# Optimization experiments

Measured on AMD Instinct MI355X. Metric: run time of the kernel, lower is better.

## Reference

```python
import jax, jax.numpy as jnp
import numpy as np

B, CTRL, KEY, MEMU = 64, 512, 64, 16384  # batch, controller_size, key_size(=memory_unit_size), memory_units
EPS_COS = 1e-8   # torch F.cosine_similarity default eps
EPS_NORM = 1e-16


def setup_inputs() -> dict:
    key = jax.random.key(0)
    ks = jax.random.split(key, 16)
    controller_state = jax.random.normal(ks[0], (B, CTRL), jnp.float32)
    pw = jax.random.uniform(ks[1], (B, MEMU), jnp.float32)
    prev_weights = pw / jnp.sum(pw, axis=1, keepdims=True)  # valid attention weights
    memory = jax.random.normal(ks[2], (B, MEMU, KEY), jnp.float32)
    def lin(k, out_d, in_d):
        kw, kb = jax.random.split(k)
        scale = 1.0 / np.sqrt(in_d)
        return (jax.random.normal(kw, (out_d, in_d), jnp.float32) * scale,
                jax.random.normal(kb, (out_d,), jnp.float32) * 0.01)
    key_W, key_b = lin(ks[3], KEY, CTRL)
    ks_W, ks_b = lin(ks[4], 1, CTRL)
    ig_W, ig_b = lin(ks[5], 1, CTRL)
    sw_W, sw_b = lin(ks[6], 3, CTRL)
    sf_W, sf_b = lin(ks[7], 1, CTRL)
    wd_W, wd_b = lin(ks[8], KEY, CTRL)
    return dict(controller_state=controller_state, prev_weights=prev_weights, memory=memory,
                key_W=key_W, key_b=key_b, ks_W=ks_W, ks_b=ks_b, ig_W=ig_W, ig_b=ig_b,
                sw_W=sw_W, sw_b=sw_b, sf_W=sf_W, sf_b=sf_b, wd_W=wd_W, wd_b=wd_b)


def _ntm_head(cs, prev_w, mem, key_W, key_b, ks_W, ks_b, ig_W, ig_b, sw_W, sw_b, sf_W, sf_b, wd_W, wd_b):
    k = cs @ key_W.T + key_b                       # (B, KEY)
    b = jax.nn.softplus(cs @ ks_W.T + ks_b)        # (B, 1) key strength
    g = jax.nn.sigmoid(cs @ ig_W.T + ig_b)         # (B, 1) interpolation gate
    s = jax.nn.softmax(cs @ sw_W.T + sw_b, axis=-1)  # (B, 3) shift weights
    y = 1.0 + jax.nn.softplus(cs @ sf_W.T + sf_b)  # (B, 1) sharpen factor
    # content addressing: softmax(b * cosine_sim(key, memory rows))
    dots = jnp.einsum('bmw,bw->bm', mem, k)        # (B, MEMU)
    denom = jnp.maximum(jnp.linalg.norm(mem, axis=2) * jnp.linalg.norm(k, axis=1, keepdims=True), EPS_COS)
    w_c = jax.nn.softmax(b * (dots / denom), axis=1)
    # interpolation with previous weights
    w_i = g * w_c + (1.0 - g) * prev_w             # (B, MEMU)
    # 3-tap circular shift (cross-correlation, matching the padded conv1d)
    shifted = (s[:, 0:1] * jnp.roll(w_i, 1, axis=1)
               + s[:, 1:2] * w_i
               + s[:, 2:3] * jnp.roll(w_i, -1, axis=1))
    # sharpen + normalize
    sharp = shifted ** y
    w = sharp / (jnp.sum(sharp, axis=1, keepdims=True) + EPS_NORM)
    data = jnp.einsum('bm,bmw->bw', w, mem)        # read mode
    return w, data


def reference(controller_state, prev_weights, memory, key_W, key_b, ks_W, ks_b,
              ig_W, ig_b, sw_W, sw_b, sf_W, sf_b, wd_W, wd_b):
    return _ntm_head(controller_state, prev_weights, memory, key_W, key_b, ks_W, ks_b,
                     ig_W, ig_b, sw_W, sw_b, sf_W, sf_b, wd_W, wd_b)
```

## Files before the change

kernel.cpp:

```cpp
#include <hip/hip_runtime.h>
#include <math.h>

#define B    64
#define CTRL 512
#define KEY  64
#define MEMU 16384

__device__ __forceinline__ float softplusf(float x) {
    return x > 20.f ? x : log1pf(expf(x));
}

__global__ __launch_bounds__(256) void k1_scalars(
    const float* __restrict__ cs,
    const float* __restrict__ key_W, const float* __restrict__ key_b,
    const float* __restrict__ ks_W,  const float* __restrict__ ks_b,
    const float* __restrict__ ig_W,  const float* __restrict__ ig_b,
    const float* __restrict__ sw_W,  const float* __restrict__ sw_b,
    const float* __restrict__ sf_W,  const float* __restrict__ sf_b,
    float* __restrict__ ws_k, float* __restrict__ ws_scal)
{
    __shared__ float cs_s[CTRL];
    __shared__ float k_s[KEY];
    __shared__ float h_s[8];
    const int b = blockIdx.x;
    const int t = threadIdx.x;
    for (int i = t; i < CTRL; i += 256) cs_s[i] = cs[b * CTRL + i];
    __syncthreads();
    const int wave = t >> 6, lane = t & 63;
    for (int o = wave; o < 70; o += 4) {
        const float* W; float bias;
        if (o < 64)       { W = key_W + o * CTRL;      bias = key_b[o]; }
        else if (o == 64) { W = ks_W;                  bias = ks_b[0]; }
        else if (o == 65) { W = ig_W;                  bias = ig_b[0]; }
        else if (o < 69)  { W = sw_W + (o - 66) * CTRL; bias = sw_b[o - 66]; }
        else              { W = sf_W;                  bias = sf_b[0]; }
        float d = 0.f;
        for (int j = lane; j < CTRL; j += 64) d += cs_s[j] * W[j];
        #pragma unroll
        for (int off = 32; off >= 1; off >>= 1) d += __shfl_xor(d, off, 64);
        if (lane == 0) {
            float r = d + bias;
            if (o < 64) { k_s[o] = r; ws_k[b * KEY + o] = r; }
            else        h_s[o - 64] = r;
        }
    }
    __syncthreads();
    if (wave == 0) {
        float kv = k_s[lane];
        float sq = kv * kv;
        #pragma unroll
        for (int off = 32; off >= 1; off >>= 1) sq += __shfl_xor(sq, off, 64);
        if (lane == 0) {
            float knorm = sqrtf(sq);
            float beta = softplusf(h_s[0]);
            float g    = 1.f / (1.f + expf(-h_s[1]));
            float m3   = fmaxf(fmaxf(h_s[2], h_s[3]), h_s[4]);
            float e0 = expf(h_s[2] - m3), e1 = expf(h_s[3] - m3), e2 = expf(h_s[4] - m3);
            float inv3 = 1.f / (e0 + e1 + e2);
            float y = 1.f + softplusf(h_s[5]);
            float* sc = ws_scal + b * 8;
            sc[0] = beta; sc[1] = g;
            sc[2] = e0 * inv3; sc[3] = e1 * inv3; sc[4] = e2 * inv3;
            sc[5] = y; sc[6] = knorm;
        }
    }
}

__global__ __launch_bounds__(256) void k2_scores(
    const float* __restrict__ mem,
    const float* __restrict__ ws_k, const float* __restrict__ ws_scal,
    float* __restrict__ ws_e, float* __restrict__ ws_pe)
{
    const int b = blockIdx.y;
    const int chunk = blockIdx.x;
    const int t = threadIdx.x;
    const float beta  = ws_scal[b * 8 + 0];
    const float knorm = ws_scal[b * 8 + 6];
    float kk[KEY];
    #pragma unroll
    for (int j = 0; j < KEY; ++j) kk[j] = ws_k[b * KEY + j];

    float esum = 0.f;
    #pragma unroll
    for (int i = 0; i < 4; ++i) {
        const int m = chunk * 1024 + i * 256 + t;
        const float4* rp = (const float4*)(mem + ((size_t)b * MEMU + m) * KEY);
        float dot = 0.f, sq = 0.f;
        #pragma unroll
        for (int q = 0; q < 16; ++q) {
            float4 v = rp[q];
            dot += v.x * kk[4*q+0] + v.y * kk[4*q+1] + v.z * kk[4*q+2] + v.w * kk[4*q+3];
            sq  += v.x * v.x + v.y * v.y + v.z * v.z + v.w * v.w;
        }
        const float denom = fmaxf(sqrtf(sq) * knorm, 1e-8f);
        const float e = expf(beta * (dot / denom) - beta);
        ws_e[b * MEMU + m] = e;
        esum += e;
    }
    __shared__ float red[4];
    #pragma unroll
    for (int off = 32; off >= 1; off >>= 1) esum += __shfl_xor(esum, off, 64);
    if ((t & 63) == 0) red[t >> 6] = esum;
    __syncthreads();
    if (t == 0) ws_pe[b * 16 + chunk] = red[0] + red[1] + red[2] + red[3];
}

__global__ __launch_bounds__(256) void k4_sharp(
    const float* __restrict__ pw,
    const float* __restrict__ ws_e, const float* __restrict__ ws_pe,
    const float* __restrict__ ws_scal,
    float* __restrict__ ws_sharp, float* __restrict__ ws_ps)
{
    const int b = blockIdx.y, chunk = blockIdx.x, t = threadIdx.x;
    float sum_e = 0.f;
    #pragma unroll
    for (int i = 0; i < 16; ++i) sum_e += ws_pe[b * 16 + i];
    const float inv_e = 1.f / sum_e;
    const float g  = ws_scal[b*8+1];
    const float s0 = ws_scal[b*8+2], s1 = ws_scal[b*8+3], s2 = ws_scal[b*8+4];
    const float y  = ws_scal[b*8+5];
    const float cg = 1.f - g;
    const float* eb = ws_e + b * MEMU;
    const float* pb = pw   + b * MEMU;

    float ssum = 0.f;
    #pragma unroll
    for (int i = 0; i < 8; ++i) {
        const int m  = chunk * 2048 + i * 256 + t;
        const int mm = (m + MEMU - 1) & (MEMU - 1);
        const int mp = (m + 1) & (MEMU - 1);
        const float wim = g * eb[mm] * inv_e + cg * pb[mm];
        const float wi0 = g * eb[m ] * inv_e + cg * pb[m ];
        const float wip = g * eb[mp] * inv_e + cg * pb[mp];
        const float sh  = s0 * wim + s1 * wi0 + s2 * wip;
        const float sp  = expf(y * logf(sh));
        ws_sharp[b * MEMU + m] = sp;
        ssum += sp;
    }
    __shared__ float red[4];
    #pragma unroll
    for (int off = 32; off >= 1; off >>= 1) ssum += __shfl_xor(ssum, off, 64);
    if ((t & 63) == 0) red[t >> 6] = ssum;
    __syncthreads();
    if (t == 0) ws_ps[b * 8 + chunk] = red[0] + red[1] + red[2] + red[3];
}

__global__ __launch_bounds__(256) void k6_wout(
    const float* __restrict__ ws_sharp, const float* __restrict__ ws_ps,
    float* __restrict__ out)
{
    const int b = blockIdx.y, chunk = blockIdx.x, t = threadIdx.x;
    float ss = 0.f;
    #pragma unroll
    for (int i = 0; i < 8; ++i) ss += ws_ps[b * 8 + i];
    const float inv = 1.f / (ss + 1e-16f);
    #pragma unroll
    for (int i = 0; i < 8; ++i) {
        const int m = chunk * 2048 + i * 256 + t;
        out[b * MEMU + m] = ws_sharp[b * MEMU + m] * inv;
    }
}

__global__ __launch_bounds__(256) void k7_data(
    const float* __restrict__ mem, const float* __restrict__ out_w,
    float* __restrict__ ws_pd)
{
    const int b = blockIdx.y, chunk = blockIdx.x;
    const int t = threadIdx.x, wave = t >> 6, lane = t & 63;
    const int r0 = chunk * 256 + wave * 64;
    const float* wb = out_w + b * MEMU;
    const float* mb = mem + (size_t)b * MEMU * KEY;
    float acc = 0.f;
    #pragma unroll 4
    for (int i = 0; i < 64; ++i) {
        const int r = r0 + i;
        acc += wb[r] * mb[(size_t)r * KEY + lane];
    }
    __shared__ float red[4][64];
    red[wave][lane] = acc;
    __syncthreads();
    if (t < 64) {
        const float s = red[0][t] + red[1][t] + red[2][t] + red[3][t];
        ws_pd[(b * 64 + chunk) * 64 + t] = s;
    }
}

__global__ __launch_bounds__(64) void k8_reduce(
    const float* __restrict__ ws_pd, float* __restrict__ out)
{
    const int b = blockIdx.x, j = threadIdx.x;
    float s = 0.f;
    #pragma unroll 8
    for (int c = 0; c < 64; ++c) s += ws_pd[(b * 64 + c) * 64 + j];
    out[(size_t)B * MEMU + b * KEY + j] = s;
}

extern "C" void kernel_launch(void* const* d_in, const int* in_sizes, int n_in,
                              void* d_out, int out_size, void* d_ws, size_t ws_size,
                              hipStream_t stream) {
    (void)in_sizes; (void)n_in; (void)out_size; (void)ws_size;
    const float* cs    = (const float*)d_in[0];
    const float* pw    = (const float*)d_in[1];
    const float* mem   = (const float*)d_in[2];
    const float* key_W = (const float*)d_in[3];
    const float* key_b = (const float*)d_in[4];
    const float* ks_W  = (const float*)d_in[5];
    const float* ks_b  = (const float*)d_in[6];
    const float* ig_W  = (const float*)d_in[7];
    const float* ig_b  = (const float*)d_in[8];
    const float* sw_W  = (const float*)d_in[9];
    const float* sw_b  = (const float*)d_in[10];
    const float* sf_W  = (const float*)d_in[11];
    const float* sf_b  = (const float*)d_in[12];
    float* out = (float*)d_out;
    float* ws  = (float*)d_ws;

    float* ws_k     = ws;
    float* ws_scal  = ws_k + B * KEY;
    float* ws_e     = ws_scal + B * 8;
    float* ws_sharp = ws_e + (size_t)B * MEMU;
    float* ws_pe    = ws_sharp + (size_t)B * MEMU;
    float* ws_ps    = ws_pe + B * 16;
    float* ws_pd    = ws_ps + B * 8;

    k1_scalars<<<dim3(B), dim3(256), 0, stream>>>(cs, key_W, key_b, ks_W, ks_b,
                                                  ig_W, ig_b, sw_W, sw_b, sf_W, sf_b,
                                                  ws_k, ws_scal);
    k2_scores<<<dim3(16, B), dim3(256), 0, stream>>>(mem, ws_k, ws_scal, ws_e, ws_pe);
    k4_sharp<<<dim3(8, B), dim3(256), 0, stream>>>(pw, ws_e, ws_pe, ws_scal, ws_sharp, ws_ps);
    k6_wout<<<dim3(8, B), dim3(256), 0, stream>>>(ws_sharp, ws_ps, out);
    k7_data<<<dim3(64, B), dim3(256), 0, stream>>>(mem, out, ws_pd);
    k8_reduce<<<dim3(B), dim3(64), 0, stream>>>(ws_pd, out);
}
```

Baseline: 125.6 us.

## Fuse weight normalization into data read kernel with float4 memory loads

```diff
diff --git a/kernel.cpp b/kernel.cpp
--- a/kernel.cpp
+++ b/kernel.cpp
@@ -145,43 +145,53 @@
     if (t == 0) ws_ps[b * 8 + chunk] = red[0] + red[1] + red[2] + red[3];
 }
 
-__global__ __launch_bounds__(256) void k6_wout(
+__global__ __launch_bounds__(256) void k7_data(
+    const float* __restrict__ mem,
     const float* __restrict__ ws_sharp, const float* __restrict__ ws_ps,
-    float* __restrict__ out)
-{
-    const int b = blockIdx.y, chunk = blockIdx.x, t = threadIdx.x;
+    float* __restrict__ out_w, float* __restrict__ ws_pd)
+{
+    const int b = blockIdx.y, chunk = blockIdx.x;
+    const int t = threadIdx.x, wv = t >> 6, lane = t & 63;
+    __shared__ float w_lds[256];
+    __shared__ float red[4][64];
+
     float ss = 0.f;
     #pragma unroll
     for (int i = 0; i < 8; ++i) ss += ws_ps[b * 8 + i];
     const float inv = 1.f / (ss + 1e-16f);
-    #pragma unroll
-    for (int i = 0; i < 8; ++i) {
-        const int m = chunk * 2048 + i * 256 + t;
-        out[b * MEMU + m] = ws_sharp[b * MEMU + m] * inv;
-    }
-}
-
-__global__ __launch_bounds__(256) void k7_data(
-    const float* __restrict__ mem, const float* __restrict__ out_w,
-    float* __restrict__ ws_pd)
-{
-    const int b = blockIdx.y, chunk = blockIdx.x;
-    const int t = threadIdx.x, wave = t >> 6, lane = t & 63;
-    const int r0 = chunk * 256 + wave * 64;
-    const float* wb = out_w + b * MEMU;
-    const float* mb = mem + (size_t)b * MEMU * KEY;
-    float acc = 0.f;
-    #pragma unroll 4
-    for (int i = 0; i < 64; ++i) {
-        const int r = r0 + i;
-        acc += wb[r] * mb[(size_t)r * KEY + lane];
-    }
-    __shared__ float red[4][64];
-    red[wave][lane] = acc;
+
+    const int m0 = chunk * 256;
+    const float wval = ws_sharp[b * MEMU + m0 + t] * inv;
+    out_w[b * MEMU + m0 + t] = wval;
+    w_lds[t] = wval;
+    __syncthreads();
+
+    const float* mb = mem + ((size_t)b * MEMU + m0 + wv * 64) * KEY;
+    const int rsub = lane >> 4;
+    const int c4   = (lane & 15) * 4;
+    float4 acc = make_float4(0.f, 0.f, 0.f, 0.f);
+    #pragma unroll
+    for (int s = 0; s < 16; ++s) {
+        const int r = s * 4 + rsub;
+        const float4 v = *(const float4*)(mb + (size_t)r * KEY + c4);
+        const float wr = w_lds[wv * 64 + r];
+        acc.x += wr * v.x; acc.y += wr * v.y; acc.z += wr * v.z; acc.w += wr * v.w;
+    }
+    #pragma unroll
+    for (int off = 16; off <= 32; off <<= 1) {
+        acc.x += __shfl_xor(acc.x, off, 64);
+        acc.y += __shfl_xor(acc.y, off, 64);
+        acc.z += __shfl_xor(acc.z, off, 64);
+        acc.w += __shfl_xor(acc.w, off, 64);
+    }
+    if (lane < 16) {
+        red[wv][c4 + 0] = acc.x; red[wv][c4 + 1] = acc.y;
+        red[wv][c4 + 2] = acc.z; red[wv][c4 + 3] = acc.w;
+    }
     __syncthreads();
     if (t < 64) {
-        const float s = red[0][t] + red[1][t] + red[2][t] + red[3][t];
-        ws_pd[(b * 64 + chunk) * 64 + t] = s;
+        ws_pd[(b * 64 + chunk) * 64 + t] =
+            red[0][t] + red[1][t] + red[2][t] + red[3][t];
     }
 }
 
@@ -228,7 +238,6 @@
                                                   ws_k, ws_scal);
     k2_scores<<<dim3(16, B), dim3(256), 0, stream>>>(mem, ws_k, ws_scal, ws_e, ws_pe);
     k4_sharp<<<dim3(8, B), dim3(256), 0, stream>>>(pw, ws_e, ws_pe, ws_scal, ws_sharp, ws_ps);
-    k6_wout<<<dim3(8, B), dim3(256), 0, stream>>>(ws_sharp, ws_ps, out);
-    k7_data<<<dim3(64, B), dim3(256), 0, stream>>>(mem, out, ws_pd);
+    k7_data<<<dim3(64, B), dim3(256), 0, stream>>>(mem, ws_sharp, ws_ps, out, ws_pd);
     k8_reduce<<<dim3(B), dim3(64), 0, stream>>>(ws_pd, out);
 }
```

After: 120.7 us. -3.9%, faster.
